# Kernel tuning notes

Hardware: AMD Instinct MI355X
Metric: run time of the kernel (lower is better)

Reference implementation:

```python
import jax, jax.numpy as jnp
import numpy as np

N_EXPERTS = 8
D_MODEL = 1024
D_FF = 4096
N_TOKENS = 2048
TOP_K = 2


def _init_expert_weight(key, shape):
    # torch init: bound = sqrt(3) * (sqrt(1/3) / sqrt(fan_in)) = 1/sqrt(fan_in), fan_in = shape[1]
    bound = 1.0 / np.sqrt(shape[1])
    return jax.random.uniform(key, shape, jnp.float32, -bound, bound)


def setup_inputs() -> dict:
    key = jax.random.key(0)
    kx, ki, kw, k1, k2, k3 = jax.random.split(key, 6)
    x = jax.random.normal(kx, (N_TOKENS, D_MODEL), jnp.float32)
    expert_indices = jax.random.randint(ki, (N_TOKENS, TOP_K), 0, N_EXPERTS, jnp.int32)
    expert_weights = jax.random.uniform(kw, (N_TOKENS, TOP_K), jnp.float32)
    w1 = _init_expert_weight(k1, (N_EXPERTS, D_MODEL, D_FF))
    w2 = _init_expert_weight(k2, (N_EXPERTS, D_MODEL, D_FF))
    w3 = _init_expert_weight(k3, (N_EXPERTS, D_FF, D_MODEL))
    return {"x": x, "expert_indices": expert_indices, "expert_weights": expert_weights,
            "w1": w1, "w2": w2, "w3": w3}


def reference(x, expert_indices, expert_weights, w1, w2, w3):
    n_tokens, d_model = x.shape
    top_k = expert_indices.shape[1]
    n_experts = w1.shape[0]
    A = n_tokens * top_k  # total assignments; static capacity per expert (no overflow possible)

    flat_e = expert_indices.reshape(-1)            # [A]
    flat_w = expert_weights.reshape(-1)            # [A]
    tok_idx = jnp.repeat(jnp.arange(n_tokens), top_k)  # [A]

    order = jnp.argsort(flat_e, stable=True)
    s_tok = tok_idx[order]
    s_e = flat_e[order]
    s_w = flat_w[order]

    counts = jnp.bincount(flat_e, length=n_experts)            # [E]
    seg_starts = jnp.concatenate([jnp.zeros((1,), counts.dtype), jnp.cumsum(counts)[:-1]])
    pos = jnp.arange(A) - seg_starts[s_e]                       # position within expert segment

    # dispatch: padded per-expert batch [E, A, d]
    padded = jnp.zeros((n_experts, A, d_model), x.dtype).at[s_e, pos].set(x[s_tok])

    gate = jax.nn.silu(jnp.einsum('ecd,edf->ecf', padded, w1))
    value = jnp.einsum('ecd,edf->ecf', padded, w2)
    hidden = gate * value
    expert_out = jnp.einsum('ecf,efd->ecd', hidden, w3)        # [E, A, d]

    # combine: gather per-assignment outputs, weight, scatter-add back to tokens
    y = expert_out[s_e, pos] * s_w[:, None]                    # [A, d]
    out = jnp.zeros((n_tokens, d_model), x.dtype).at[s_tok].add(y)
    return out
```

## Files before the change

kernel.cpp:

```cpp
#include <hip/hip_runtime.h>
#include <stdint.h>

#define N_EXPERTS 8
#define D_MODEL 1024
#define D_FF 4096
#define N_TOKENS 2048
#define ASSN 4096
#define ROWS 4224
#define BK 32
#define SKB 36

using bfrag = __attribute__((ext_vector_type(8))) short;
using f32x4 = __attribute__((ext_vector_type(4))) float;
typedef unsigned short u16;

__device__ __forceinline__ u16 f2bf(float f) {
  uint32_t u = __builtin_bit_cast(uint32_t, f);
  u += 0x7fffu + ((u >> 16) & 1u);
  return (u16)(u >> 16);
}

__device__ __forceinline__ void gll16(const void* g, void* l) {
  __builtin_amdgcn_global_load_lds(
      (const __attribute__((address_space(1))) void*)g,
      (__attribute__((address_space(3))) void*)l, 16, 0, 0);
}

__device__ __forceinline__ bfrag ldb64x2(const u16* p) {
  union { bfrag f; uint2 u[2]; } t;
  t.u[0] = *(const uint2*)p;
  t.u[1] = *(const uint2*)(p + 4);
  return t.f;
}
__device__ __forceinline__ void stb64x2(u16* p, bfrag f) {
  union { bfrag f; uint2 u[2]; } t; t.f = f;
  *(uint2*)p = t.u[0];
  *(uint2*)(p + 4) = t.u[1];
}

__global__ void k_setup(const int* __restrict__ eidx, const float* __restrict__ ew,
                        int* __restrict__ rowmap, int* __restrict__ arow,
                        int* __restrict__ counts, int* __restrict__ offs) {
  __shared__ int sc[N_EXPERTS], so[N_EXPERTS];
  int t = threadIdx.x;
  if (t < N_EXPERTS) sc[t] = 0;
  __syncthreads();
  for (int a = t; a < ASSN; a += 256) atomicAdd(&sc[eidx[a]], 1);
  __syncthreads();
  if (t == 0) {
    int run = 0;
    for (int e = 0; e < N_EXPERTS; e++) {
      counts[e] = sc[e]; offs[e] = run; so[e] = run; run += sc[e];
    }
  }
  __syncthreads();
  for (int a = t; a < ASSN; a += 256) {
    int e = eidx[a];
    int p = atomicAdd(&so[e], 1);
    rowmap[p] = a;
    arow[a] = p;
  }
}

__global__ void k_gather(const float* __restrict__ x, const int* __restrict__ rowmap,
                         u16* __restrict__ Xg) {
  int r = blockIdx.x, t = threadIdx.x;
  uint2 o;
  if (r < ASSN) {
    int tok = rowmap[r] >> 1;
    float4 v = *(const float4*)(x + (size_t)tok * D_MODEL + t * 4);
    o.x = (uint32_t)f2bf(v.x) | ((uint32_t)f2bf(v.y) << 16);
    o.y = (uint32_t)f2bf(v.z) | ((uint32_t)f2bf(v.w) << 16);
  } else {
    o.x = 0u; o.y = 0u;
  }
  *(uint2*)(Xg + (size_t)r * D_MODEL + t * 4) = o;
}

__launch_bounds__(256, 2)
__global__ void k_gemm1(const u16* __restrict__ Xg,
                        const float* __restrict__ w1, const float* __restrict__ w2,
                        const int* __restrict__ counts, const int* __restrict__ offs,
                        u16* __restrict__ H) {
  const int e = blockIdx.z, nt = blockIdx.x, mt = blockIdx.y;
  const int cnt = counts[e];
  if (mt * 128 >= cnt) return;
  const int row0 = offs[e] + mt * 128;
  const int mrem = cnt - mt * 128;
  const int n0 = nt * 128;

  __shared__ u16 As[2][128 * BK];
  __shared__ u16 Bs1[2][128 * SKB];
  __shared__ u16 Bs2[2][128 * SKB];

  const int tid = threadIdx.x;
  const int lane = tid & 63, wave = tid >> 6;
  const int wm = (wave >> 1) << 6, wn = (wave & 1) << 6;
  const int l16 = lane & 15, quad = lane >> 4;

  const int off0 = (tid >> 2) * D_MODEL + (tid & 3) * 8;
  const int off1 = off0 + 64 * D_MODEL;
  const int ldso = wave * 512;

  const u16* gA = Xg + (size_t)row0 * D_MODEL;

  const int n2 = lane * 2;
  const int kh = wave * 8;
  const float* pB1 = w1 + (size_t)e * D_MODEL * D_FF + (size_t)kh * D_FF + n0 + n2;
  const float* pB2 = w2 + (size_t)e * D_MODEL * D_FF + (size_t)kh * D_FF + n0 + n2;
  const size_t bstep = (size_t)BK * D_FF;

  f32x4 acc1[4][4] = {};
  f32x4 acc2[4][4] = {};

  float2 v1[8], v2[8];
  #pragma unroll
  for (int kk = 0; kk < 8; kk++) {
    v1[kk] = *(const float2*)(pB1 + (size_t)kk * D_FF);
    v2[kk] = *(const float2*)(pB2 + (size_t)kk * D_FF);
  }
  pB1 += bstep; pB2 += bstep;
  gll16(gA + off0, &As[0][ldso]);
  gll16(gA + off1, &As[0][ldso + 2048]);
  {
    bfrag p0, p1;
    #pragma unroll
    for (int kk = 0; kk < 8; kk++) { p0[kk] = (short)f2bf(v1[kk].x); p1[kk] = (short)f2bf(v1[kk].y); }
    *(bfrag*)&Bs1[0][n2 * SKB + kh] = p0;
    stb64x2(&Bs1[0][(n2 + 1) * SKB + kh], p1);
    #pragma unroll
    for (int kk = 0; kk < 8; kk++) { p0[kk] = (short)f2bf(v2[kk].x); p1[kk] = (short)f2bf(v2[kk].y); }
    *(bfrag*)&Bs2[0][n2 * SKB + kh] = p0;
    stb64x2(&Bs2[0][(n2 + 1) * SKB + kh], p1);
  }
  #pragma unroll
  for (int kk = 0; kk < 8; kk++) {
    v1[kk] = *(const float2*)(pB1 + (size_t)kk * D_FF);
    v2[kk] = *(const float2*)(pB2 + (size_t)kk * D_FF);
  }
  pB1 += bstep; pB2 += bstep;
  __syncthreads();

  const u16* gAn = gA + BK;
  #pragma unroll 2
  for (int ks = 0; ks < 32; ks++) {
    const int c = ks & 1;
    if (ks < 31) {
      gll16(gAn + off0, &As[1 - c][ldso]);
      gll16(gAn + off1, &As[1 - c][ldso + 2048]);
      gAn += BK;
      bfrag p0, p1;
      #pragma unroll
      for (int kk = 0; kk < 8; kk++) { p0[kk] = (short)f2bf(v1[kk].x); p1[kk] = (short)f2bf(v1[kk].y); }
      *(bfrag*)&Bs1[1 - c][n2 * SKB + kh] = p0;
      stb64x2(&Bs1[1 - c][(n2 + 1) * SKB + kh], p1);
      #pragma unroll
      for (int kk = 0; kk < 8; kk++) { p0[kk] = (short)f2bf(v2[kk].x); p1[kk] = (short)f2bf(v2[kk].y); }
      *(bfrag*)&Bs2[1 - c][n2 * SKB + kh] = p0;
      stb64x2(&Bs2[1 - c][(n2 + 1) * SKB + kh], p1);
      if (ks < 30) {
        #pragma unroll
        for (int kk = 0; kk < 8; kk++) {
          v1[kk] = *(const float2*)(pB1 + (size_t)kk * D_FF);
          v2[kk] = *(const float2*)(pB2 + (size_t)kk * D_FF);
        }
        pB1 += bstep; pB2 += bstep;
      }
    }
    bfrag b1[4], b2[4];
    #pragma unroll
    for (int j = 0; j < 4; j++) {
      b1[j] = ldb64x2(&Bs1[c][(wn + j * 16 + l16) * SKB + quad * 8]);
      b2[j] = ldb64x2(&Bs2[c][(wn + j * 16 + l16) * SKB + quad * 8]);
    }
    #pragma unroll
    for (int i = 0; i < 4; i++) {
      bfrag a = *(const bfrag*)&As[c][(wm + i * 16 + l16) * BK + quad * 8];
      #pragma unroll
      for (int j = 0; j < 4; j++) {
        acc1[i][j] = __builtin_amdgcn_mfma_f32_16x16x32_bf16(a, b1[j], acc1[i][j], 0, 0, 0);
        acc2[i][j] = __builtin_amdgcn_mfma_f32_16x16x32_bf16(a, b2[j], acc2[i][j], 0, 0, 0);
      }
    }
    __syncthreads();
  }

  #pragma unroll
  for (int i = 0; i < 4; i++) {
    #pragma unroll
    for (int p = 0; p < 4; p++) {
      const int mloc = wm + i * 16 + quad * 4 + p;
      if (mloc < mrem) {
        u16* dst = H + (size_t)(row0 + mloc) * D_FF + n0 + wn + l16;
        #pragma unroll
        for (int j = 0; j < 4; j++) {
          float g = acc1[i][j][p];
          float vv = acc2[i][j][p];
          float h = g / (1.0f + __expf(-g)) * vv;
          dst[j * 16] = f2bf(h);
        }
      }
    }
  }
}

__launch_bounds__(256, 2)
__global__ void k_gemm2(const u16* __restrict__ H, const float* __restrict__ w3,
                        const int* __restrict__ counts, const int* __restrict__ offs,
                        float* __restrict__ Y0, float* __restrict__ Y1) {
  const int e = blockIdx.z >> 1, khalf = blockIdx.z & 1;
  const int nt = blockIdx.x, mt = blockIdx.y;
  const int cnt = counts[e];
  if (mt * 128 >= cnt) return;
  const int row0 = offs[e] + mt * 128;
  const int mrem = cnt - mt * 128;
  const int n0 = nt * 128;
  float* __restrict__ Y = khalf ? Y1 : Y0;

  __shared__ u16 As[2][128 * BK];
  __shared__ u16 Bs[2][128 * SKB];

  const int tid = threadIdx.x;
  const int lane = tid & 63, wave = tid >> 6;
  const int wm = (wave >> 1) << 6, wn = (wave & 1) << 6;
  const int l16 = lane & 15, quad = lane >> 4;

  const int off0 = (tid >> 2) * D_FF + (tid & 3) * 8;
  const int off1 = off0 + 64 * D_FF;
  const int ldso = wave * 512;

  const u16* gA = H + (size_t)row0 * D_FF + khalf * 2048;

  const int n2 = lane * 2;
  const int kh = wave * 8;
  const float* pB = w3 + (size_t)e * D_FF * D_MODEL
                  + (size_t)(khalf * 2048 + kh) * D_MODEL + n0 + n2;
  const size_t bstep = (size_t)BK * D_MODEL;

  f32x4 acc[4][4] = {};

  float2 v[8];
  #pragma unroll
  for (int kk = 0; kk < 8; kk++) v[kk] = *(const float2*)(pB + (size_t)kk * D_MODEL);
  pB += bstep;
  gll16(gA + off0, &As[0][ldso]);
  gll16(gA + off1, &As[0][ldso + 2048]);
  {
    bfrag p0, p1;
    #pragma unroll
    for (int kk = 0; kk < 8; kk++) { p0[kk] = (short)f2bf(v[kk].x); p1[kk] = (short)f2bf(v[kk].y); }
    *(bfrag*)&Bs[0][n2 * SKB + kh] = p0;
    stb64x2(&Bs[0][(n2 + 1) * SKB + kh], p1);
  }
  #pragma unroll
  for (int kk = 0; kk < 8; kk++) v[kk] = *(const float2*)(pB + (size_t)kk * D_MODEL);
  pB += bstep;
  __syncthreads();

  const u16* gAn = gA + BK;
  #pragma unroll 2
  for (int ks = 0; ks < 64; ks++) {
    const int c = ks & 1;
    if (ks < 63) {
      gll16(gAn + off0, &As[1 - c][ldso]);
      gll16(gAn + off1, &As[1 - c][ldso + 2048]);
      gAn += BK;
      bfrag p0, p1;
      #pragma unroll
      for (int kk = 0; kk < 8; kk++) { p0[kk] = (short)f2bf(v[kk].x); p1[kk] = (short)f2bf(v[kk].y); }
      *(bfrag*)&Bs[1 - c][n2 * SKB + kh] = p0;
      stb64x2(&Bs[1 - c][(n2 + 1) * SKB + kh], p1);
      if (ks < 62) {
        #pragma unroll
        for (int kk = 0; kk < 8; kk++) v[kk] = *(const float2*)(pB + (size_t)kk * D_MODEL);
        pB += bstep;
      }
    }
    bfrag b[4];
    #pragma unroll
    for (int j = 0; j < 4; j++)
      b[j] = ldb64x2(&Bs[c][(wn + j * 16 + l16) * SKB + quad * 8]);
    #pragma unroll
    for (int i = 0; i < 4; i++) {
      bfrag a = *(const bfrag*)&As[c][(wm + i * 16 + l16) * BK + quad * 8];
      #pragma unroll
      for (int j = 0; j < 4; j++)
        acc[i][j] = __builtin_amdgcn_mfma_f32_16x16x32_bf16(a, b[j], acc[i][j], 0, 0, 0);
    }
    __syncthreads();
  }

  #pragma unroll
  for (int i = 0; i < 4; i++) {
    #pragma unroll
    for (int p = 0; p < 4; p++) {
      const int mloc = wm + i * 16 + quad * 4 + p;
      if (mloc < mrem) {
        float* dst = Y + (size_t)(row0 + mloc) * D_MODEL + n0 + wn + l16;
        #pragma unroll
        for (int j = 0; j < 4; j++) dst[j * 16] = acc[i][j][p];
      }
    }
  }
}

__global__ void k_combine(const float* __restrict__ Y0, const float* __restrict__ Y1,
                          const int* __restrict__ arow, const float* __restrict__ ew,
                          float* __restrict__ out) {
  const int tk = blockIdx.x;
  const int d = threadIdx.x * 4;
  const int a0 = tk * 2, a1 = tk * 2 + 1;
  const int r0 = arow[a0], r1 = arow[a1];
  const float w0 = ew[a0], w1 = ew[a1];
  const float4 p0 = *(const float4*)(Y0 + (size_t)r0 * D_MODEL + d);
  const float4 q0 = *(const float4*)(Y1 + (size_t)r0 * D_MODEL + d);
  const float4 p1 = *(const float4*)(Y0 + (size_t)r1 * D_MODEL + d);
  const float4 q1 = *(const float4*)(Y1 + (size_t)r1 * D_MODEL + d);
  float4 r;
  r.x = w0 * (p0.x + q0.x) + w1 * (p1.x + q1.x);
  r.y = w0 * (p0.y + q0.y) + w1 * (p1.y + q1.y);
  r.z = w0 * (p0.z + q0.z) + w1 * (p1.z + q1.z);
  r.w = w0 * (p0.w + q0.w) + w1 * (p1.w + q1.w);
  *(float4*)(out + (size_t)tk * D_MODEL + d) = r;
}

extern "C" void kernel_launch(void* const* d_in, const int* in_sizes, int n_in,
                              void* d_out, int out_size, void* d_ws, size_t ws_size,
                              hipStream_t stream) {
  const float* x  = (const float*)d_in[0];
  const int* eidx = (const int*)d_in[1];
  const float* ew = (const float*)d_in[2];
  const float* w1 = (const float*)d_in[3];
  const float* w2 = (const float*)d_in[4];
  const float* w3 = (const float*)d_in[5];
  float* out = (float*)d_out;

  char* ws = (char*)d_ws;
  int*   rowmap = (int*)(ws);
  int*   arow   = (int*)(ws + 16384);
  int*   counts = (int*)(ws + 32768);
  int*   offs   = (int*)(ws + 32768 + 64);
  const size_t D0 = 65536;
  const size_t SZ_XG = (size_t)ROWS * D_MODEL * 2;
  const size_t SZ_HB = (size_t)ROWS * D_FF * 2;
  const size_t SZ_Y  = (size_t)ROWS * D_MODEL * 4;
  u16*   Xg = (u16*)(ws + D0);
  u16*   Hb = (u16*)(ws + D0 + SZ_XG);
  float* Y0 = (float*)(ws + D0 + SZ_XG + SZ_HB);
  float* Y1 = (float*)(ws + D0 + SZ_XG + SZ_HB + SZ_Y);

  k_setup<<<1, 256, 0, stream>>>(eidx, ew, rowmap, arow, counts, offs);
  k_gather<<<ROWS, 256, 0, stream>>>(x, rowmap, Xg);
  k_gemm1<<<dim3(D_FF / 128, 32, N_EXPERTS), 256, 0, stream>>>(Xg, w1, w2, counts, offs, Hb);
  k_gemm2<<<dim3(D_MODEL / 128, 32, N_EXPERTS * 2), 256, 0, stream>>>(Hb, w3, counts, offs, Y0, Y1);
  k_combine<<<N_TOKENS, 256, 0, stream>>>(Y0, Y1, arow, ew, out);
}
```

Measured before the change: 620.6 us.

## Pre-convert expert weights to transposed bf16 and stream both GEMM operands via LDS DMA

Adds a k_convt kernel that converts each expert's fp32 weight matrix to bf16 and transposes it to N-major (K contiguous) layout in workspace before each GEMM. Both GEMMs then load A and B tiles with global_load_lds directly into unpadded LDS, which removes the per-iteration register-staged fp32 loads, conversions and strided LDS stores inside the main loop. The cost is three extra passes that read all fp32 weights and write bf16 copies every call, and the w3 copy reuses the w1 buffer. The unpadded B layout may also bring LDS bank conflicts.

```diff
diff --git a/kernel.cpp b/kernel.cpp
--- a/kernel.cpp
+++ b/kernel.cpp
@@ -8,7 +8,6 @@
 #define ASSN 4096
 #define ROWS 4224
 #define BK 32
-#define SKB 36
 
 using bfrag = __attribute__((ext_vector_type(8))) short;
 using f32x4 = __attribute__((ext_vector_type(4))) float;
@@ -24,18 +23,6 @@
   __builtin_amdgcn_global_load_lds(
       (const __attribute__((address_space(1))) void*)g,
       (__attribute__((address_space(3))) void*)l, 16, 0, 0);
-}
-
-__device__ __forceinline__ bfrag ldb64x2(const u16* p) {
-  union { bfrag f; uint2 u[2]; } t;
-  t.u[0] = *(const uint2*)p;
-  t.u[1] = *(const uint2*)(p + 4);
-  return t.f;
-}
-__device__ __forceinline__ void stb64x2(u16* p, bfrag f) {
-  union { bfrag f; uint2 u[2]; } t; t.f = f;
-  *(uint2*)p = t.u[0];
-  *(uint2*)(p + 4) = t.u[1];
 }
 
 __global__ void k_setup(const int* __restrict__ eidx, const float* __restrict__ ew,
@@ -77,9 +64,38 @@
   *(uint2*)(Xg + (size_t)r * D_MODEL + t * 4) = o;
 }
 
+__global__ void k_convt(const float* __restrict__ src, u16* __restrict__ dst,
+                        int K, int N) {
+  const int e = blockIdx.y;
+  src += (size_t)e * K * N;
+  dst += (size_t)e * K * N;
+  const int ntn = N >> 6;
+  const int n0 = (blockIdx.x % ntn) << 6;
+  const int k0 = (blockIdx.x / ntn) << 7;
+  __shared__ u16 T[64][136];
+  const int t = threadIdx.x;
+  const int rk = t >> 4, rn4 = (t & 15) << 2;
+  #pragma unroll
+  for (int p = 0; p < 8; p++) {
+    const int k = rk + p * 16;
+    float4 v = *(const float4*)(src + (size_t)(k0 + k) * N + n0 + rn4);
+    T[rn4 + 0][k] = f2bf(v.x);
+    T[rn4 + 1][k] = f2bf(v.y);
+    T[rn4 + 2][k] = f2bf(v.z);
+    T[rn4 + 3][k] = f2bf(v.w);
+  }
+  __syncthreads();
+  const int wn = t >> 4, wk8 = (t & 15) << 3;
+  #pragma unroll
+  for (int p = 0; p < 4; p++) {
+    const int n = wn + p * 16;
+    *(bfrag*)(dst + (size_t)(n0 + n) * K + k0 + wk8) = *(const bfrag*)&T[n][wk8];
+  }
+}
+
 __launch_bounds__(256, 2)
 __global__ void k_gemm1(const u16* __restrict__ Xg,
-                        const float* __restrict__ w1, const float* __restrict__ w2,
+                        const u16* __restrict__ w1t, const u16* __restrict__ w2t,
                         const int* __restrict__ counts, const int* __restrict__ offs,
                         u16* __restrict__ H) {
   const int e = blockIdx.z, nt = blockIdx.x, mt = blockIdx.y;
@@ -90,88 +106,52 @@
   const int n0 = nt * 128;
 
   __shared__ u16 As[2][128 * BK];
-  __shared__ u16 Bs1[2][128 * SKB];
-  __shared__ u16 Bs2[2][128 * SKB];
+  __shared__ u16 B1s[2][128 * BK];
+  __shared__ u16 B2s[2][128 * BK];
 
   const int tid = threadIdx.x;
   const int lane = tid & 63, wave = tid >> 6;
   const int wm = (wave >> 1) << 6, wn = (wave & 1) << 6;
   const int l16 = lane & 15, quad = lane >> 4;
 
-  const int off0 = (tid >> 2) * D_MODEL + (tid & 3) * 8;
-  const int off1 = off0 + 64 * D_MODEL;
-  const int ldso = wave * 512;
-
-  const u16* gA = Xg + (size_t)row0 * D_MODEL;
-
-  const int n2 = lane * 2;
-  const int kh = wave * 8;
-  const float* pB1 = w1 + (size_t)e * D_MODEL * D_FF + (size_t)kh * D_FF + n0 + n2;
-  const float* pB2 = w2 + (size_t)e * D_MODEL * D_FF + (size_t)kh * D_FF + n0 + n2;
-  const size_t bstep = (size_t)BK * D_FF;
+  const int srow = wave * 32 + (lane >> 2);
+  const int scol = (lane & 3) * 8;
+  const int ld0 = wave * 1024;
+
+  const u16* pA  = Xg  + (size_t)(row0 + srow) * D_MODEL + scol;
+  const u16* pB1 = w1t + (size_t)e * D_MODEL * D_FF + (size_t)(n0 + srow) * D_MODEL + scol;
+  const u16* pB2 = w2t + (size_t)e * D_MODEL * D_FF + (size_t)(n0 + srow) * D_MODEL + scol;
+  const size_t rstep = (size_t)16 * D_MODEL;
 
   f32x4 acc1[4][4] = {};
   f32x4 acc2[4][4] = {};
 
-  float2 v1[8], v2[8];
-  #pragma unroll
-  for (int kk = 0; kk < 8; kk++) {
-    v1[kk] = *(const float2*)(pB1 + (size_t)kk * D_FF);
-    v2[kk] = *(const float2*)(pB2 + (size_t)kk * D_FF);
-  }
-  pB1 += bstep; pB2 += bstep;
-  gll16(gA + off0, &As[0][ldso]);
-  gll16(gA + off1, &As[0][ldso + 2048]);
-  {
-    bfrag p0, p1;
-    #pragma unroll
-    for (int kk = 0; kk < 8; kk++) { p0[kk] = (short)f2bf(v1[kk].x); p1[kk] = (short)f2bf(v1[kk].y); }
-    *(bfrag*)&Bs1[0][n2 * SKB + kh] = p0;
-    stb64x2(&Bs1[0][(n2 + 1) * SKB + kh], p1);
-    #pragma unroll
-    for (int kk = 0; kk < 8; kk++) { p0[kk] = (short)f2bf(v2[kk].x); p1[kk] = (short)f2bf(v2[kk].y); }
-    *(bfrag*)&Bs2[0][n2 * SKB + kh] = p0;
-    stb64x2(&Bs2[0][(n2 + 1) * SKB + kh], p1);
-  }
-  #pragma unroll
-  for (int kk = 0; kk < 8; kk++) {
-    v1[kk] = *(const float2*)(pB1 + (size_t)kk * D_FF);
-    v2[kk] = *(const float2*)(pB2 + (size_t)kk * D_FF);
-  }
-  pB1 += bstep; pB2 += bstep;
-  __syncthreads();
-
-  const u16* gAn = gA + BK;
+  gll16(pA,          &As[0][ld0]);
+  gll16(pA + rstep,  &As[0][ld0 + 512]);
+  gll16(pB1,         &B1s[0][ld0]);
+  gll16(pB1 + rstep, &B1s[0][ld0 + 512]);
+  gll16(pB2,         &B2s[0][ld0]);
+  gll16(pB2 + rstep, &B2s[0][ld0 + 512]);
+  pA += BK; pB1 += BK; pB2 += BK;
+  __syncthreads();
+
   #pragma unroll 2
   for (int ks = 0; ks < 32; ks++) {
     const int c = ks & 1;
     if (ks < 31) {
-      gll16(gAn + off0, &As[1 - c][ldso]);
-      gll16(gAn + off1, &As[1 - c][ldso + 2048]);
-      gAn += BK;
-      bfrag p0, p1;
-      #pragma unroll
-      for (int kk = 0; kk < 8; kk++) { p0[kk] = (short)f2bf(v1[kk].x); p1[kk] = (short)f2bf(v1[kk].y); }
-      *(bfrag*)&Bs1[1 - c][n2 * SKB + kh] = p0;
-      stb64x2(&Bs1[1 - c][(n2 + 1) * SKB + kh], p1);
-      #pragma unroll
-      for (int kk = 0; kk < 8; kk++) { p0[kk] = (short)f2bf(v2[kk].x); p1[kk] = (short)f2bf(v2[kk].y); }
-      *(bfrag*)&Bs2[1 - c][n2 * SKB + kh] = p0;
-      stb64x2(&Bs2[1 - c][(n2 + 1) * SKB + kh], p1);
-      if (ks < 30) {
-        #pragma unroll
-        for (int kk = 0; kk < 8; kk++) {
-          v1[kk] = *(const float2*)(pB1 + (size_t)kk * D_FF);
-          v2[kk] = *(const float2*)(pB2 + (size_t)kk * D_FF);
-        }
-        pB1 += bstep; pB2 += bstep;
-      }
+      gll16(pA,          &As[1 - c][ld0]);
+      gll16(pA + rstep,  &As[1 - c][ld0 + 512]);
+      gll16(pB1,         &B1s[1 - c][ld0]);
+      gll16(pB1 + rstep, &B1s[1 - c][ld0 + 512]);
+      gll16(pB2,         &B2s[1 - c][ld0]);
+      gll16(pB2 + rstep, &B2s[1 - c][ld0 + 512]);
+      pA += BK; pB1 += BK; pB2 += BK;
     }
     bfrag b1[4], b2[4];
     #pragma unroll
     for (int j = 0; j < 4; j++) {
-      b1[j] = ldb64x2(&Bs1[c][(wn + j * 16 + l16) * SKB + quad * 8]);
-      b2[j] = ldb64x2(&Bs2[c][(wn + j * 16 + l16) * SKB + quad * 8]);
+      b1[j] = *(const bfrag*)&B1s[c][(wn + j * 16 + l16) * BK + quad * 8];
+      b2[j] = *(const bfrag*)&B2s[c][(wn + j * 16 + l16) * BK + quad * 8];
     }
     #pragma unroll
     for (int i = 0; i < 4; i++) {
@@ -205,7 +185,7 @@
 }
 
 __launch_bounds__(256, 2)
-__global__ void k_gemm2(const u16* __restrict__ H, const float* __restrict__ w3,
+__global__ void k_gemm2(const u16* __restrict__ H, const u16* __restrict__ w3t,
                         const int* __restrict__ counts, const int* __restrict__ offs,
                         float* __restrict__ Y0, float* __restrict__ Y1) {
   const int e = blockIdx.z >> 1, khalf = blockIdx.z & 1;
@@ -218,68 +198,45 @@
   float* __restrict__ Y = khalf ? Y1 : Y0;
 
   __shared__ u16 As[2][128 * BK];
-  __shared__ u16 Bs[2][128 * SKB];
+  __shared__ u16 Bs[2][128 * BK];
 
   const int tid = threadIdx.x;
   const int lane = tid & 63, wave = tid >> 6;
   const int wm = (wave >> 1) << 6, wn = (wave & 1) << 6;
   const int l16 = lane & 15, quad = lane >> 4;
 
-  const int off0 = (tid >> 2) * D_FF + (tid & 3) * 8;
-  const int off1 = off0 + 64 * D_FF;
-  const int ldso = wave * 512;
-
-  const u16* gA = H + (size_t)row0 * D_FF + khalf * 2048;
-
-  const int n2 = lane * 2;
-  const int kh = wave * 8;
-  const float* pB = w3 + (size_t)e * D_FF * D_MODEL
-                  + (size_t)(khalf * 2048 + kh) * D_MODEL + n0 + n2;
-  const size_t bstep = (size_t)BK * D_MODEL;
+  const int srow = wave * 32 + (lane >> 2);
+  const int scol = (lane & 3) * 8;
+  const int ld0 = wave * 1024;
+
+  const u16* pA = H + (size_t)(row0 + srow) * D_FF + khalf * 2048 + scol;
+  const u16* pB = w3t + (size_t)e * D_FF * D_MODEL
+                + (size_t)(n0 + srow) * D_FF + khalf * 2048 + scol;
+  const size_t rstepA = (size_t)16 * D_FF;
 
   f32x4 acc[4][4] = {};
 
-  float2 v[8];
-  #pragma unroll
-  for (int kk = 0; kk < 8; kk++) v[kk] = *(const float2*)(pB + (size_t)kk * D_MODEL);
-  pB += bstep;
-  gll16(gA + off0, &As[0][ldso]);
-  gll16(gA + off1, &As[0][ldso + 2048]);
-  {
-    bfrag p0, p1;
-    #pragma unroll
-    for (int kk = 0; kk < 8; kk++) { p0[kk] = (short)f2bf(v[kk].x); p1[kk] = (short)f2bf(v[kk].y); }
-    *(bfrag*)&Bs[0][n2 * SKB + kh] = p0;
-    stb64x2(&Bs[0][(n2 + 1) * SKB + kh], p1);
-  }
-  #pragma unroll
-  for (int kk = 0; kk < 8; kk++) v[kk] = *(const float2*)(pB + (size_t)kk * D_MODEL);
-  pB += bstep;
-  __syncthreads();
-
-  const u16* gAn = gA + BK;
+  gll16(pA,           &As[0][ld0]);
+  gll16(pA + rstepA,  &As[0][ld0 + 512]);
+  gll16(pB,           &Bs[0][ld0]);
+  gll16(pB + rstepA,  &Bs[0][ld0 + 512]);
+  pA += BK; pB += BK;
+  __syncthreads();
+
   #pragma unroll 2
   for (int ks = 0; ks < 64; ks++) {
     const int c = ks & 1;
     if (ks < 63) {
-      gll16(gAn + off0, &As[1 - c][ldso]);
-      gll16(gAn + off1, &As[1 - c][ldso + 2048]);
-      gAn += BK;
-      bfrag p0, p1;
-      #pragma unroll
-      for (int kk = 0; kk < 8; kk++) { p0[kk] = (short)f2bf(v[kk].x); p1[kk] = (short)f2bf(v[kk].y); }
-      *(bfrag*)&Bs[1 - c][n2 * SKB + kh] = p0;
-      stb64x2(&Bs[1 - c][(n2 + 1) * SKB + kh], p1);
-      if (ks < 62) {
-        #pragma unroll
-        for (int kk = 0; kk < 8; kk++) v[kk] = *(const float2*)(pB + (size_t)kk * D_MODEL);
-        pB += bstep;
-      }
+      gll16(pA,          &As[1 - c][ld0]);
+      gll16(pA + rstepA, &As[1 - c][ld0 + 512]);
+      gll16(pB,          &Bs[1 - c][ld0]);
+      gll16(pB + rstepA, &Bs[1 - c][ld0 + 512]);
+      pA += BK; pB += BK;
     }
     bfrag b[4];
     #pragma unroll
     for (int j = 0; j < 4; j++)
-      b[j] = ldb64x2(&Bs[c][(wn + j * 16 + l16) * SKB + quad * 8]);
+      b[j] = *(const bfrag*)&Bs[c][(wn + j * 16 + l16) * BK + quad * 8];
     #pragma unroll
     for (int i = 0; i < 4; i++) {
       bfrag a = *(const bfrag*)&As[c][(wm + i * 16 + l16) * BK + quad * 8];
@@ -344,14 +301,21 @@
   const size_t SZ_XG = (size_t)ROWS * D_MODEL * 2;
   const size_t SZ_HB = (size_t)ROWS * D_FF * 2;
   const size_t SZ_Y  = (size_t)ROWS * D_MODEL * 4;
-  u16*   Xg = (u16*)(ws + D0);
-  u16*   Hb = (u16*)(ws + D0 + SZ_XG);
-  float* Y0 = (float*)(ws + D0 + SZ_XG + SZ_HB);
-  float* Y1 = (float*)(ws + D0 + SZ_XG + SZ_HB + SZ_Y);
+  const size_t SZ_W  = (size_t)N_EXPERTS * D_MODEL * D_FF * 2;
+  u16*   Xg  = (u16*)(ws + D0);
+  u16*   Hb  = (u16*)(ws + D0 + SZ_XG);
+  float* Y0  = (float*)(ws + D0 + SZ_XG + SZ_HB);
+  float* Y1  = (float*)(ws + D0 + SZ_XG + SZ_HB + SZ_Y);
+  u16*   wt1 = (u16*)(ws + D0 + SZ_XG + SZ_HB + 2 * SZ_Y);
+  u16*   wt2 = wt1 + SZ_W / 2;
+  u16*   wt3 = wt1;
 
   k_setup<<<1, 256, 0, stream>>>(eidx, ew, rowmap, arow, counts, offs);
   k_gather<<<ROWS, 256, 0, stream>>>(x, rowmap, Xg);
-  k_gemm1<<<dim3(D_FF / 128, 32, N_EXPERTS), 256, 0, stream>>>(Xg, w1, w2, counts, offs, Hb);
-  k_gemm2<<<dim3(D_MODEL / 128, 32, N_EXPERTS * 2), 256, 0, stream>>>(Hb, w3, counts, offs, Y0, Y1);
+  k_convt<<<dim3(512, N_EXPERTS), 256, 0, stream>>>(w1, wt1, D_MODEL, D_FF);
+  k_convt<<<dim3(512, N_EXPERTS), 256, 0, stream>>>(w2, wt2, D_MODEL, D_FF);
+  k_gemm1<<<dim3(D_FF / 128, 32, N_EXPERTS), 256, 0, stream>>>(Xg, wt1, wt2, counts, offs, Hb);
+  k_convt<<<dim3(512, N_EXPERTS), 256, 0, stream>>>(w3, wt3, D_FF, D_MODEL);
+  k_gemm2<<<dim3(D_MODEL / 128, 32, N_EXPERTS * 2), 256, 0, stream>>>(Hb, wt3, counts, offs, Y0, Y1);
   k_combine<<<N_TOKENS, 256, 0, stream>>>(Y0, Y1, arow, ew, out);
 }
```

New measurement: 622.7 us. No clear change (+0.3%).
